# Kernel tuning notes

Measured on AMD Instinct MI355X. Metric: run time of the kernel, lower is better.

## Reference

```python
import jax, jax.numpy as jnp
import numpy as np

GRID = 64
DX = 1.0 / GRID            # grid spacing (buffer dx)
RADIUS = 2.5 * DX          # search_radius = dx * 2.5
CIN, COUT = 16, 16
B, N = 2, 8192
EPS = 1e-12
FOUR_OVER_PI = 4.0 / np.pi


def _safe_sqrt(v):
    return jnp.sqrt(jnp.maximum(v, EPS))


def _sphere_to_cylinder(x, y, z):
    # volume-preserving map: unit ball -> cylinder (radius 1, height 2)
    sq = x * x + y * y + z * z
    norm = _safe_sqrt(sq)
    xy2 = x * x + y * y
    cap = 1.25 * z * z > xy2                      # polar-cap region
    s_cap = jnp.sqrt(3.0 * norm / (norm + jnp.abs(z) + EPS))
    s_side = norm / _safe_sqrt(xy2)
    xc = jnp.where(cap, x * s_cap, x * s_side)
    yc = jnp.where(cap, y * s_cap, y * s_side)
    zc = jnp.where(cap, jnp.sign(z) * norm, 1.5 * z)
    zero = sq <= EPS
    z0 = jnp.zeros_like(x)
    return (jnp.where(zero, z0, xc), jnp.where(zero, z0, yc), jnp.where(zero, z0, zc))


def _cylinder_to_cube(x, y, z):
    # area-preserving disc -> square on the xy cross-section
    xy2 = x * x + y * y
    nxy = _safe_sqrt(xy2)
    xdom = jnp.abs(y) <= jnp.abs(x)
    safe_x = jnp.where(jnp.abs(x) > EPS, x, 1.0)
    safe_y = jnp.where(jnp.abs(y) > EPS, y, 1.0)
    tx = jnp.sign(x) * nxy
    ty = jnp.sign(y) * nxy
    xa, ya = tx, tx * FOUR_OVER_PI * jnp.arctan(y / safe_x)
    xb, yb = ty * FOUR_OVER_PI * jnp.arctan(x / safe_y), ty
    xc = jnp.where(xdom, xa, xb)
    yc = jnp.where(xdom, ya, yb)
    zero = xy2 <= EPS
    z0 = jnp.zeros_like(x)
    return jnp.where(zero, z0, xc), jnp.where(zero, z0, yc), z


def _cconv_forward(input, pos, weights, grid_pos):
    Bb, C, D, H, Wd = input.shape
    Np = pos.shape[1]
    # [B,C,D,H,W] -> [B,D,H,W,C] -> [B,G,C]  (matches permute+view in torch)
    feat = jnp.transpose(input, (0, 2, 3, 4, 1)).reshape(Bb, D * H * Wd, C)
    # fixed 6^3 stencil of candidate grid cells around each point
    off = jnp.arange(6) - 2
    o0, o1, o2 = jnp.meshgrid(off, off, off, indexing='ij')
    offs = jnp.stack([o0, o1, o2], axis=-1).reshape(-1, 3)          # [216,3]
    base = jnp.floor(pos / DX).astype(jnp.int32)                    # [B,N,3]
    cand = base[:, :, None, :] + offs[None, None]                   # [B,N,216,3]
    dims = jnp.array([D, H, Wd])
    in_bounds = jnp.all((cand >= 0) & (cand < dims), axis=-1)       # [B,N,216]
    cc = jnp.clip(cand, 0, dims - 1)
    flat = (cc[..., 0] * H + cc[..., 1]) * Wd + cc[..., 2]          # [B,N,216]
    bidx = jnp.arange(Bb)[:, None, None]
    npos = grid_pos[flat]                                           # [B,N,216,3]
    fg = feat[bidx, flat]                                           # [B,N,216,C]
    rel = npos - pos[:, :, None, :]
    dist2 = jnp.sum(rel * rel, axis=-1)
    valid = in_bounds & (dist2 <= RADIUS * RADIUS)
    # map relative offsets (scaled to the unit ball) to the unit cube
    u = rel / RADIUS
    x, y, z = _sphere_to_cylinder(u[..., 0], u[..., 1], u[..., 2])
    x, y, z = _cylinder_to_cube(x, y, z)
    # linear interpolation of the 3x3x3 kernel, align_corners=True -> coords in [0,2]
    taps = jnp.arange(3, dtype=pos.dtype)
    def hat(c):
        c = jnp.clip((c * 0.5 + 0.5) * 2.0, 0.0, 2.0)
        return jnp.maximum(0.0, 1.0 - jnp.abs(c[..., None] - taps))  # [B,N,216,3]
    w0, w1, w2 = hat(x), hat(y), hat(z)
    w27 = jnp.einsum('bnki,bnkj,bnkl->bnkijl', w0, w1, w2).reshape(Bb, Np, -1, 27)
    w27 = w27 * valid[..., None].astype(w27.dtype)
    # accumulate interpolated features per kernel tap, then apply the kernel
    acc = jnp.einsum('bnkt,bnkc->bntc', w27, fg)                    # [B,N,27,C]
    out = jnp.einsum('bntc,tcd->bnd', acc, weights.reshape(27, C, -1))
    # normalize=True (Open3D default): divide by neighbor count
    count = jnp.sum(valid, axis=-1).astype(out.dtype)
    out = out / jnp.maximum(count, 1.0)[..., None]
    return out


def setup_inputs() -> dict:
    key = jax.random.key(0)
    k1, k2, k3 = jax.random.split(key, 3)
    inp = jax.random.normal(k1, (B, CIN, GRID, GRID, GRID), jnp.float32)
    pos = jax.random.uniform(k2, (B, N, 3), jnp.float32)
    weights = jax.random.normal(k3, (3, 3, 3, CIN, COUT), jnp.float32) * 0.05
    ax = jnp.arange(GRID, dtype=jnp.float32) * DX
    g = jnp.stack(jnp.meshgrid(ax, ax, ax, indexing='ij'), axis=-1).reshape(-1, 3)
    return {"input": inp, "pos": pos, "weights": weights, "grid_pos": g}


def reference(input, pos, weights, grid_pos):
    return _cconv_forward(input, pos, weights, grid_pos)
```

## Files before the change

### kernel.cpp

```cpp
#include <hip/hip_runtime.h>
#include <cstdint>

typedef float v2f __attribute__((ext_vector_type(2)));

namespace {
constexpr int kG = 262144;
constexpr int kB = 2;
constexpr int kN = 8192;
constexpr int kPts = kB * kN;
constexpr float kDX = 1.0f / 64.0f;
constexpr float kRad2 = 0.00152587890625f;
constexpr float kInvRad = 25.6f;
constexpr float kEps = 1e-12f;
constexpr float kFourOverPi = 1.27323954473516268615f;

constexpr int PPB = 4;
constexpr int THREADS = PPB * 64;
constexpr int MAXREC = 96;
constexpr int SLOT = 12;
constexpr int NFLAT = 96;
constexpr int GSTRIDE = MAXREC * SLOT + NFLAT;
}

struct Stencil {
    int v[192];
    constexpr Stencil() : v() {
        int n = 0;
        for (int a = 0; a < 6; ++a)
            for (int b = 0; b < 6; ++b)
                for (int c = 0; c < 6; ++c) {
                    int e = ((a == 0) | (a == 5)) + ((b == 0) | (b == 5)) +
                            ((c == 0) | (c == 5));
                    if (e < 2) { v[n] = a | (b << 8) | (c << 16); ++n; }
                }
        for (; n < 192; ++n) v[n] = 0x7F7F7F;
    }
};
__device__ constexpr Stencil kStencil{};

__device__ __forceinline__ float sgnf(float v) {
    return (v > 0.f) ? 1.f : ((v < 0.f) ? -1.f : 0.f);
}

__global__ __launch_bounds__(256) void transpose_feat_k(const float* __restrict__ in,
                                                        float* __restrict__ feat) {
    int idx = blockIdx.x * 256 + threadIdx.x;
    if (idx >= kB * kG) return;
    int b = idx >> 18;
    int g = idx & (kG - 1);
    float v[16];
#pragma unroll
    for (int c = 0; c < 16; ++c) v[c] = in[((size_t)(b * 16 + c)) * kG + g];
    float4* dst = reinterpret_cast<float4*>(feat + (size_t)idx * 16);
    dst[0] = make_float4(v[0], v[1], v[2], v[3]);
    dst[1] = make_float4(v[4], v[5], v[6], v[7]);
    dst[2] = make_float4(v[8], v[9], v[10], v[11]);
    dst[3] = make_float4(v[12], v[13], v[14], v[15]);
}

template <int USE_FEAT>
__global__ __launch_bounds__(THREADS) void cconv_main(
    const float* __restrict__ input, const float* __restrict__ pos,
    const float* __restrict__ W, const float* __restrict__ feat,
    float* __restrict__ out)
{
    __shared__ __align__(16) float rec[PPB * GSTRIDE];

    const int tid = threadIdx.x;
    const int wv = tid >> 6;
    const int lane = tid & 63;
    const int sg = lane >> 4;
    const int lig = lane & 15;
    const int pt = blockIdx.x * PPB + wv;
    const int b = pt >> 13;

    const float px = pos[pt * 3 + 0];
    const float py = pos[pt * 3 + 1];
    const float pz = pos[pt * 3 + 2];
    const int bx = (int)floorf(px * 64.f);
    const int by = (int)floorf(py * 64.f);
    const int bz = (int)floorf(pz * 64.f);

    float* grec = rec + wv * GSTRIDE;
    int* iflats = reinterpret_cast<int*>(grec + MAXREC * SLOT);
    int nv = 0;

#pragma unroll
    for (int it = 0; it < 3; ++it) {
        int k = it * 64 + lane;
        int pk = kStencil.v[k];
        int a = pk & 0xFF, b1 = (pk >> 8) & 0xFF, c1 = pk >> 16;
        int g0 = bx + a - 2, g1 = by + b1 - 2, g2 = bz + c1 - 2;
        bool inb = (g0 >= 0) & (g0 < 64) & (g1 >= 0) & (g1 < 64) &
                   (g2 >= 0) & (g2 < 64);
        int q0 = min(max(g0, 0), 63);
        int q1 = min(max(g1, 0), 63);
        int q2 = min(max(g2, 0), 63);
        int flat16 = ((q0 * 64 + q1) * 64 + q2) << 4;
        float rx = __fsub_rn((float)q0 * kDX, px);
        float ry = __fsub_rn((float)q1 * kDX, py);
        float rz = __fsub_rn((float)q2 * kDX, pz);
        float d2 = __fadd_rn(__fadd_rn(__fmul_rn(rx, rx), __fmul_rn(ry, ry)),
                             __fmul_rn(rz, rz));
        bool valid = inb && (d2 <= kRad2);
        unsigned long long ball = __ballot(valid);
        if (valid) {
            int slot = nv + __popcll(ball & ((1ull << lane) - 1ull));
            *reinterpret_cast<float4*>(grec + slot * SLOT) =
                make_float4(rx, ry, rz, 0.f);
            iflats[slot] = flat16;
        }
        nv += (int)__popcll(ball);
    }
    __builtin_amdgcn_wave_barrier();

    for (int z = nv + lane; z < MAXREC; z += 64) {
        float4 zf = make_float4(0.f, 0.f, 0.f, 0.f);
        float4* zp = reinterpret_cast<float4*>(grec + z * SLOT);
        zp[0] = zf; zp[1] = zf; zp[2] = zf;
        iflats[z] = 0;
    }
    __builtin_amdgcn_wave_barrier();

    const float* fbp = USE_FEAT ? (feat + (size_t)b * kG * 16)
                                : (input + (size_t)b * 16 * kG);
#define LDF(IDX) (USE_FEAT ? fbp[(size_t)iflats[(IDX)] + lig]                 \
                           : fbp[(size_t)lig * kG + (iflats[(IDX)] >> 4)])
    float fa0 = LDF(sg),      fa1 = LDF(sg + 4);
    float fa2 = LDF(sg + 8),  fa3 = LDF(sg + 12);
    float fb0 = LDF(sg + 16), fb1 = LDF(sg + 20);
    float fb2 = LDF(sg + 24), fb3 = LDF(sg + 28);

    for (int s = lane; s < nv; s += 64) {
        float* rp = grec + s * SLOT;
        float4 rc = *reinterpret_cast<const float4*>(rp);
        float ux = rc.x * kInvRad, uy = rc.y * kInvRad, uz = rc.z * kInvRad;

        float xx = ux * ux, yy = uy * uy, zz = uz * uz;
        float xy2 = xx + yy;
        float sq = xy2 + zz;
        float nrm = __builtin_amdgcn_sqrtf(fmaxf(sq, kEps));
        bool cap = (1.25f * zz > xy2);
        float scap = __builtin_amdgcn_sqrtf(3.f * nrm) *
                     __builtin_amdgcn_rsqf(nrm + fabsf(uz) + kEps);
        float sside = nrm * __builtin_amdgcn_rsqf(fmaxf(xy2, kEps));
        float sc = cap ? scap : sside;
        float xc = ux * sc, yc = uy * sc;
        float zc = cap ? sgnf(uz) * nrm : 1.5f * uz;
        if (sq <= kEps) { xc = 0.f; yc = 0.f; zc = 0.f; }

        float xy2b = xc * xc + yc * yc;
        float nxy = __builtin_amdgcn_sqrtf(fmaxf(xy2b, kEps));
        bool xdom = (fabsf(yc) <= fabsf(xc));
        float num = xdom ? yc : xc;
        float den = xdom ? xc : yc;
        float dsafe = (fabsf(den) > kEps) ? den : 1.0f;
        float r = num * __builtin_amdgcn_rcpf(dsafe);
        float r2 = r * r;
        float at = -0.01172120f;
        at = at * r2 + 0.05265332f;
        at = at * r2 - 0.11643287f;
        at = at * r2 + 0.19354346f;
        at = at * r2 - 0.33262347f;
        at = at * r2 + 0.99997726f;
        at = at * r;
        float tt = sgnf(den) * nxy;
        float g = tt * kFourOverPi * at;
        float xo = xdom ? tt : g;
        float yo = xdom ? g : tt;
        if (xy2b <= kEps) { xo = 0.f; yo = 0.f; }
        float zo = zc;

        float tx = fminf(fmaxf(xo + 1.f, 0.f), 2.f) - 1.f;
        float ty = fminf(fmaxf(yo + 1.f, 0.f), 2.f) - 1.f;
        float tz = fminf(fmaxf(zo + 1.f, 0.f), 2.f) - 1.f;
        float wx0 = fmaxf(0.f, -tx), wx1 = 1.f - fabsf(tx), wx2 = fmaxf(0.f, tx);
        float wy0 = fmaxf(0.f, -ty), wy1 = 1.f - fabsf(ty), wy2 = fmaxf(0.f, ty);
        float wz0 = fmaxf(0.f, -tz), wz1 = 1.f - fabsf(tz);

        float4* rp4 = reinterpret_cast<float4*>(rp);
        rp4[0] = make_float4(wx0 * wy0, wx0 * wy1, wx0 * wy2, wx1 * wy0);
        rp4[1] = make_float4(wx1 * wy1, wx1 * wy2, wx2 * wy0, wx2 * wy1);
        rp4[2] = make_float4(wx2 * wy2, wz0, wz1, 0.f);
    }
    __builtin_amdgcn_wave_barrier();

    v2f az0_01 = {0.f, 0.f}, az1_01 = {0.f, 0.f}, az2_01 = {0.f, 0.f};
    v2f az0_23 = {0.f, 0.f}, az1_23 = {0.f, 0.f}, az2_23 = {0.f, 0.f};
    v2f az0_45 = {0.f, 0.f}, az1_45 = {0.f, 0.f}, az2_45 = {0.f, 0.f};
    v2f az0_67 = {0.f, 0.f}, az1_67 = {0.f, 0.f}, az2_67 = {0.f, 0.f};
    float a8_0 = 0.f, a8_1 = 0.f, a8_2 = 0.f;

    const int R = (nv + 7) & ~7;
    const int F = R >> 4;
    const bool HB = (R & 8) != 0;

#define REC_FMA(S, FV)                                                        \
  {                                                                           \
    const float4* rp4_ = reinterpret_cast<const float4*>(grec + (S) * SLOT);  \
    float4 Wa = rp4_[0], Wb = rp4_[1], Wc = rp4_[2];                          \
    float m0 = Wc.y * (FV), m1 = Wc.z * (FV);                                 \
    float m2 = ((1.f - Wc.y) - Wc.z) * (FV);                                  \
    v2f mz0 = {m0, m0}, mz1 = {m1, m1}, mz2 = {m2, m2};                       \
    v2f p01 = {Wa.x, Wa.y}, p23 = {Wa.z, Wa.w};                               \
    v2f p45 = {Wb.x, Wb.y}, p67 = {Wb.z, Wb.w};                               \
    az0_01 = __builtin_elementwise_fma(p01, mz0, az0_01);                     \
    az1_01 = __builtin_elementwise_fma(p01, mz1, az1_01);                     \
    az2_01 = __builtin_elementwise_fma(p01, mz2, az2_01);                     \
    az0_23 = __builtin_elementwise_fma(p23, mz0, az0_23);                     \
    az1_23 = __builtin_elementwise_fma(p23, mz1, az1_23);                     \
    az2_23 = __builtin_elementwise_fma(p23, mz2, az2_23);                     \
    az0_45 = __builtin_elementwise_fma(p45, mz0, az0_45);                     \
    az1_45 = __builtin_elementwise_fma(p45, mz1, az1_45);                     \
    az2_45 = __builtin_elementwise_fma(p45, mz2, az2_45);                     \
    az0_67 = __builtin_elementwise_fma(p67, mz0, az0_67);                     \
    az1_67 = __builtin_elementwise_fma(p67, mz1, az1_67);                     \
    az2_67 = __builtin_elementwise_fma(p67, mz2, az2_67);                     \
    a8_0 = __builtin_fmaf(Wc.x, m0, a8_0);                                    \
    a8_1 = __builtin_fmaf(Wc.x, m1, a8_1);                                    \
    a8_2 = __builtin_fmaf(Wc.x, m2, a8_2);                                    \
  }

#define P2BODY(KK, F0_, F1_, F2_, F3_)                                        \
  {                                                                           \
    const int rb_ = (KK) * 16 + sg;                                           \
    const bool nxt_ = ((KK) + 2 < F) || ((KK) + 2 == F && HB);                \
    float n0_ = 0.f, n1_ = 0.f, n2_ = 0.f, n3_ = 0.f;                         \
    if (nxt_) {                                                               \
      n0_ = LDF(rb_ + 32); n1_ = LDF(rb_ + 36);                               \
      n2_ = LDF(rb_ + 40); n3_ = LDF(rb_ + 44);                               \
    }                                                                         \
    REC_FMA(rb_, F0_); REC_FMA(rb_ + 4, F1_);                                 \
    if ((KK) < F) { REC_FMA(rb_ + 8, F2_); REC_FMA(rb_ + 12, F3_); }          \
    if (nxt_) { F0_ = n0_; F1_ = n1_; F2_ = n2_; F3_ = n3_; }                 \
  }

     P2BODY(0, fa0, fa1, fa2, fa3)
    if (1 < F || (1 == F && HB)) P2BODY(1, fb0, fb1, fb2, fb3)
    if (2 < F || (2 == F && HB)) P2BODY(2, fa0, fa1, fa2, fa3)
    if (3 < F || (3 == F && HB)) P2BODY(3, fb0, fb1, fb2, fb3)
    if (4 < F || (4 == F && HB)) P2BODY(4, fa0, fa1, fa2, fa3)
    if (5 == F && HB)            P2BODY(5, fb0, fb1, fb2, fb3)

    float acc[28] = {
        az0_01.x, az1_01.x, az2_01.x,
        az0_01.y, az1_01.y, az2_01.y,
        az0_23.x, az1_23.x, az2_23.x,
        az0_23.y, az1_23.y, az2_23.y,
        az0_45.x, az1_45.x, az2_45.x,
        az0_45.y, az1_45.y, az2_45.y,
        az0_67.x, az1_67.x, az2_67.x,
        az0_67.y, az1_67.y, az2_67.y,
        a8_0,     a8_1,     a8_2,
        0.f
    };

    const bool hi32 = (lane >= 32);
    float kp[14];
#pragma unroll
    for (int j = 0; j < 14; ++j) {
        float send = hi32 ? acc[j] : acc[14 + j];
        float recv = __shfl_xor(send, 32);
        kp[j] = (hi32 ? acc[14 + j] : acc[j]) + recv;
    }
    const bool hi16 = (lane & 16) != 0;
    float kk[7];
#pragma unroll
    for (int j = 0; j < 7; ++j) {
        float send = hi16 ? kp[j] : kp[7 + j];
        float recv = __shfl_xor(send, 16);
        kk[j] = (hi16 ? kp[7 + j] : kp[j]) + recv;
    }

    float partial[16];
#pragma unroll
    for (int d = 0; d < 16; ++d) partial[d] = 0.f;
    const float* wbase = W + (sg * 7) * 256 + lig * 16;
#pragma unroll
    for (int j = 0; j < 7; ++j) {
        if (sg * 7 + j < 27) {
            const float4* wr = reinterpret_cast<const float4*>(wbase + j * 256);
            float4 a0 = wr[0], a1 = wr[1], a2 = wr[2], a3 = wr[3];
            float at_ = kk[j];
            partial[0]  += at_ * a0.x; partial[1]  += at_ * a0.y;
            partial[2]  += at_ * a0.z; partial[3]  += at_ * a0.w;
            partial[4]  += at_ * a1.x; partial[5]  += at_ * a1.y;
            partial[6]  += at_ * a1.z; partial[7]  += at_ * a1.w;
            partial[8]  += at_ * a2.x; partial[9]  += at_ * a2.y;
            partial[10] += at_ * a2.z; partial[11] += at_ * a2.w;
            partial[12] += at_ * a3.x; partial[13] += at_ * a3.y;
            partial[14] += at_ * a3.z; partial[15] += at_ * a3.w;
        }
    }

#pragma unroll
    for (int half = 8; half >= 1; half >>= 1) {
        bool up = (lig & half) != 0;
#pragma unroll
        for (int j = 0; j < half; ++j) {
            float send = up ? partial[j] : partial[j + half];
            float recv = __shfl_xor(send, half);
            partial[j] = (up ? partial[j + half] : partial[j]) + recv;
        }
    }
    float res = partial[0];
    res += __shfl_xor(res, 16);
    res += __shfl_xor(res, 32);
    res = res / fmaxf((float)nv, 1.f);
    if (lane < 16) out[(size_t)pt * 16 + lig] = res;
#undef LDF
#undef REC_FMA
#undef P2BODY
}

extern "C" void kernel_launch(void* const* d_in, const int* in_sizes, int n_in,
                              void* d_out, int out_size, void* d_ws, size_t ws_size,
                              hipStream_t stream) {
    const float* input = (const float*)d_in[0];
    const float* pos   = (const float*)d_in[1];
    const float* W     = (const float*)d_in[2];
    float* out  = (float*)d_out;
    float* feat = (float*)d_ws;

    const size_t feat_bytes = (size_t)kB * kG * 16 * sizeof(float);
    int use_feat = (d_ws != nullptr && ws_size >= feat_bytes) ? 1 : 0;

    if (use_feat) {
        transpose_feat_k<<<(kB * kG + 255) / 256, 256, 0, stream>>>(input, feat);
        cconv_main<1><<<kPts / PPB, THREADS, 0, stream>>>(input, pos, W, feat, out);
    } else {
        cconv_main<0><<<kPts / PPB, THREADS, 0, stream>>>(input, pos, W, feat, out);
    }
}
```

Baseline: 73.83 us.

## Remap lanes to 8 cells x 8 channel-pairs with v2f loads and reductions

Changes the per-wave thread mapping from 4 cells x 16 channels to 8 cells x 8 channel pairs. Each lane now loads two adjacent channels as a v2f and accumulates 27 taps for both with packed FMAs. The cross-lane reduction tree and the final weight contraction are rewritten to match, using v2f shuffles and channel-pair weight loads. This aims to halve the number of record passes per cell and make better use of packed math, at the cost of more accumulator registers (54 floats) and a more complex reduction with more shuffles.

```diff
diff --git a/kernel.cpp b/kernel.cpp
--- a/kernel.cpp
+++ b/kernel.cpp
@@ -42,6 +42,13 @@
     return (v > 0.f) ? 1.f : ((v < 0.f) ? -1.f : 0.f);
 }
 
+__device__ __forceinline__ v2f shfl2(v2f v, int m) {
+    v2f r;
+    r.x = __shfl_xor(v.x, m);
+    r.y = __shfl_xor(v.y, m);
+    return r;
+}
+
 __global__ __launch_bounds__(256) void transpose_feat_k(const float* __restrict__ in,
                                                         float* __restrict__ feat) {
     int idx = blockIdx.x * 256 + threadIdx.x;
@@ -69,8 +76,6 @@
     const int tid = threadIdx.x;
     const int wv = tid >> 6;
     const int lane = tid & 63;
-    const int sg = lane >> 4;
-    const int lig = lane & 15;
     const int pt = blockIdx.x * PPB + wv;
     const int b = pt >> 13;
 
@@ -122,14 +127,21 @@
     }
     __builtin_amdgcn_wave_barrier();
 
+    const int cell = lane >> 3;
+    const int cg = lane & 7;
+
     const float* fbp = USE_FEAT ? (feat + (size_t)b * kG * 16)
                                 : (input + (size_t)b * 16 * kG);
-#define LDF(IDX) (USE_FEAT ? fbp[(size_t)iflats[(IDX)] + lig]                 \
-                           : fbp[(size_t)lig * kG + (iflats[(IDX)] >> 4)])
-    float fa0 = LDF(sg),      fa1 = LDF(sg + 4);
-    float fa2 = LDF(sg + 8),  fa3 = LDF(sg + 12);
-    float fb0 = LDF(sg + 16), fb1 = LDF(sg + 20);
-    float fb2 = LDF(sg + 24), fb3 = LDF(sg + 28);
+#define LDF2v(FL)                                                             \
+    (USE_FEAT                                                                 \
+         ? *reinterpret_cast<const v2f*>(fbp + (size_t)(FL) + 2 * cg)         \
+         : (v2f){fbp[(size_t)(2 * cg) * kG + ((FL) >> 4)],                    \
+                 fbp[(size_t)(2 * cg + 1) * kG + ((FL) >> 4)]})
+
+    v2f fA = LDF2v(iflats[cell]);
+    v2f fB = LDF2v(iflats[8 + cell]);
+    v2f fC = LDF2v(iflats[16 + cell]);
+    v2f fD = LDF2v(iflats[24 + cell]);
 
     for (int s = lane; s < nv; s += 64) {
         float* rp = grec + s * SLOT;
@@ -185,131 +197,142 @@
     }
     __builtin_amdgcn_wave_barrier();
 
-    v2f az0_01 = {0.f, 0.f}, az1_01 = {0.f, 0.f}, az2_01 = {0.f, 0.f};
-    v2f az0_23 = {0.f, 0.f}, az1_23 = {0.f, 0.f}, az2_23 = {0.f, 0.f};
-    v2f az0_45 = {0.f, 0.f}, az1_45 = {0.f, 0.f}, az2_45 = {0.f, 0.f};
-    v2f az0_67 = {0.f, 0.f}, az1_67 = {0.f, 0.f}, az2_67 = {0.f, 0.f};
-    float a8_0 = 0.f, a8_1 = 0.f, a8_2 = 0.f;
-
-    const int R = (nv + 7) & ~7;
-    const int F = R >> 4;
-    const bool HB = (R & 8) != 0;
-
-#define REC_FMA(S, FV)                                                        \
+    v2f acc[32];
+#pragma unroll
+    for (int t = 0; t < 32; ++t) acc[t] = (v2f){0.f, 0.f};
+
+#define REC_FMA2(RPTR, FV)                                                    \
   {                                                                           \
-    const float4* rp4_ = reinterpret_cast<const float4*>(grec + (S) * SLOT);  \
+    const float4* rp4_ = reinterpret_cast<const float4*>(RPTR);               \
     float4 Wa = rp4_[0], Wb = rp4_[1], Wc = rp4_[2];                          \
-    float m0 = Wc.y * (FV), m1 = Wc.z * (FV);                                 \
-    float m2 = ((1.f - Wc.y) - Wc.z) * (FV);                                  \
-    v2f mz0 = {m0, m0}, mz1 = {m1, m1}, mz2 = {m2, m2};                       \
-    v2f p01 = {Wa.x, Wa.y}, p23 = {Wa.z, Wa.w};                               \
-    v2f p45 = {Wb.x, Wb.y}, p67 = {Wb.z, Wb.w};                               \
-    az0_01 = __builtin_elementwise_fma(p01, mz0, az0_01);                     \
-    az1_01 = __builtin_elementwise_fma(p01, mz1, az1_01);                     \
-    az2_01 = __builtin_elementwise_fma(p01, mz2, az2_01);                     \
-    az0_23 = __builtin_elementwise_fma(p23, mz0, az0_23);                     \
-    az1_23 = __builtin_elementwise_fma(p23, mz1, az1_23);                     \
-    az2_23 = __builtin_elementwise_fma(p23, mz2, az2_23);                     \
-    az0_45 = __builtin_elementwise_fma(p45, mz0, az0_45);                     \
-    az1_45 = __builtin_elementwise_fma(p45, mz1, az1_45);                     \
-    az2_45 = __builtin_elementwise_fma(p45, mz2, az2_45);                     \
-    az0_67 = __builtin_elementwise_fma(p67, mz0, az0_67);                     \
-    az1_67 = __builtin_elementwise_fma(p67, mz1, az1_67);                     \
-    az2_67 = __builtin_elementwise_fma(p67, mz2, az2_67);                     \
-    a8_0 = __builtin_fmaf(Wc.x, m0, a8_0);                                    \
-    a8_1 = __builtin_fmaf(Wc.x, m1, a8_1);                                    \
-    a8_2 = __builtin_fmaf(Wc.x, m2, a8_2);                                    \
+    v2f m0 = (v2f){Wc.y, Wc.y} * (FV);                                        \
+    v2f m1 = (v2f){Wc.z, Wc.z} * (FV);                                        \
+    float wz2_ = (1.f - Wc.y) - Wc.z;                                         \
+    v2f m2 = (v2f){wz2_, wz2_} * (FV);                                        \
+    acc[0]  = __builtin_elementwise_fma((v2f){Wa.x, Wa.x}, m0, acc[0]);       \
+    acc[1]  = __builtin_elementwise_fma((v2f){Wa.x, Wa.x}, m1, acc[1]);       \
+    acc[2]  = __builtin_elementwise_fma((v2f){Wa.x, Wa.x}, m2, acc[2]);       \
+    acc[3]  = __builtin_elementwise_fma((v2f){Wa.y, Wa.y}, m0, acc[3]);       \
+    acc[4]  = __builtin_elementwise_fma((v2f){Wa.y, Wa.y}, m1, acc[4]);       \
+    acc[5]  = __builtin_elementwise_fma((v2f){Wa.y, Wa.y}, m2, acc[5]);       \
+    acc[6]  = __builtin_elementwise_fma((v2f){Wa.z, Wa.z}, m0, acc[6]);       \
+    acc[7]  = __builtin_elementwise_fma((v2f){Wa.z, Wa.z}, m1, acc[7]);       \
+    acc[8]  = __builtin_elementwise_fma((v2f){Wa.z, Wa.z}, m2, acc[8]);       \
+    acc[9]  = __builtin_elementwise_fma((v2f){Wa.w, Wa.w}, m0, acc[9]);       \
+    acc[10] = __builtin_elementwise_fma((v2f){Wa.w, Wa.w}, m1, acc[10]);      \
+    acc[11] = __builtin_elementwise_fma((v2f){Wa.w, Wa.w}, m2, acc[11]);      \
+    acc[12] = __builtin_elementwise_fma((v2f){Wb.x, Wb.x}, m0, acc[12]);      \
+    acc[13] = __builtin_elementwise_fma((v2f){Wb.x, Wb.x}, m1, acc[13]);      \
+    acc[14] = __builtin_elementwise_fma((v2f){Wb.x, Wb.x}, m2, acc[14]);      \
+    acc[15] = __builtin_elementwise_fma((v2f){Wb.y, Wb.y}, m0, acc[15]);      \
+    acc[16] = __builtin_elementwise_fma((v2f){Wb.y, Wb.y}, m1, acc[16]);      \
+    acc[17] = __builtin_elementwise_fma((v2f){Wb.y, Wb.y}, m2, acc[17]);      \
+    acc[18] = __builtin_elementwise_fma((v2f){Wb.z, Wb.z}, m0, acc[18]);      \
+    acc[19] = __builtin_elementwise_fma((v2f){Wb.z, Wb.z}, m1, acc[19]);      \
+    acc[20] = __builtin_elementwise_fma((v2f){Wb.z, Wb.z}, m2, acc[20]);      \
+    acc[21] = __builtin_elementwise_fma((v2f){Wb.w, Wb.w}, m0, acc[21]);      \
+    acc[22] = __builtin_elementwise_fma((v2f){Wb.w, Wb.w}, m1, acc[22]);      \
+    acc[23] = __builtin_elementwise_fma((v2f){Wb.w, Wb.w}, m2, acc[23]);      \
+    acc[24] = __builtin_elementwise_fma((v2f){Wc.x, Wc.x}, m0, acc[24]);      \
+    acc[25] = __builtin_elementwise_fma((v2f){Wc.x, Wc.x}, m1, acc[25]);      \
+    acc[26] = __builtin_elementwise_fma((v2f){Wc.x, Wc.x}, m2, acc[26]);      \
   }
 
-#define P2BODY(KK, F0_, F1_, F2_, F3_)                                        \
-  {                                                                           \
-    const int rb_ = (KK) * 16 + sg;                                           \
-    const bool nxt_ = ((KK) + 2 < F) || ((KK) + 2 == F && HB);                \
-    float n0_ = 0.f, n1_ = 0.f, n2_ = 0.f, n3_ = 0.f;                         \
-    if (nxt_) {                                                               \
-      n0_ = LDF(rb_ + 32); n1_ = LDF(rb_ + 36);                               \
-      n2_ = LDF(rb_ + 40); n3_ = LDF(rb_ + 44);                               \
-    }                                                                         \
-    REC_FMA(rb_, F0_); REC_FMA(rb_ + 4, F1_);                                 \
-    if ((KK) < F) { REC_FMA(rb_ + 8, F2_); REC_FMA(rb_ + 12, F3_); }          \
-    if (nxt_) { F0_ = n0_; F1_ = n1_; F2_ = n2_; F3_ = n3_; }                 \
+#define P2BODY(KK, FCUR)                                                      \
+  if ((KK) * 8 < nv) {                                                        \
+    v2f fn_ = FCUR;                                                           \
+    if (((KK) + 4) * 8 < nv) fn_ = LDF2v(iflats[((KK) + 4) * 8 + cell]);      \
+    REC_FMA2(grec + ((KK) * 8 + cell) * SLOT, FCUR);                          \
+    FCUR = fn_;                                                               \
   }
 
-     P2BODY(0, fa0, fa1, fa2, fa3)
-    if (1 < F || (1 == F && HB)) P2BODY(1, fb0, fb1, fb2, fb3)
-    if (2 < F || (2 == F && HB)) P2BODY(2, fa0, fa1, fa2, fa3)
-    if (3 < F || (3 == F && HB)) P2BODY(3, fb0, fb1, fb2, fb3)
-    if (4 < F || (4 == F && HB)) P2BODY(4, fa0, fa1, fa2, fa3)
-    if (5 == F && HB)            P2BODY(5, fb0, fb1, fb2, fb3)
-
-    float acc[28] = {
-        az0_01.x, az1_01.x, az2_01.x,
-        az0_01.y, az1_01.y, az2_01.y,
-        az0_23.x, az1_23.x, az2_23.x,
-        az0_23.y, az1_23.y, az2_23.y,
-        az0_45.x, az1_45.x, az2_45.x,
-        az0_45.y, az1_45.y, az2_45.y,
-        az0_67.x, az1_67.x, az2_67.x,
-        az0_67.y, az1_67.y, az2_67.y,
-        a8_0,     a8_1,     a8_2,
-        0.f
-    };
-
-    const bool hi32 = (lane >= 32);
-    float kp[14];
-#pragma unroll
-    for (int j = 0; j < 14; ++j) {
-        float send = hi32 ? acc[j] : acc[14 + j];
-        float recv = __shfl_xor(send, 32);
-        kp[j] = (hi32 ? acc[14 + j] : acc[j]) + recv;
-    }
-    const bool hi16 = (lane & 16) != 0;
-    float kk[7];
-#pragma unroll
-    for (int j = 0; j < 7; ++j) {
-        float send = hi16 ? kp[j] : kp[7 + j];
-        float recv = __shfl_xor(send, 16);
-        kk[j] = (hi16 ? kp[7 + j] : kp[j]) + recv;
-    }
-
-    float partial[16];
-#pragma unroll
-    for (int d = 0; d < 16; ++d) partial[d] = 0.f;
-    const float* wbase = W + (sg * 7) * 256 + lig * 16;
-#pragma unroll
-    for (int j = 0; j < 7; ++j) {
-        if (sg * 7 + j < 27) {
-            const float4* wr = reinterpret_cast<const float4*>(wbase + j * 256);
-            float4 a0 = wr[0], a1 = wr[1], a2 = wr[2], a3 = wr[3];
-            float at_ = kk[j];
-            partial[0]  += at_ * a0.x; partial[1]  += at_ * a0.y;
-            partial[2]  += at_ * a0.z; partial[3]  += at_ * a0.w;
-            partial[4]  += at_ * a1.x; partial[5]  += at_ * a1.y;
-            partial[6]  += at_ * a1.z; partial[7]  += at_ * a1.w;
-            partial[8]  += at_ * a2.x; partial[9]  += at_ * a2.y;
-            partial[10] += at_ * a2.z; partial[11] += at_ * a2.w;
-            partial[12] += at_ * a3.x; partial[13] += at_ * a3.y;
-            partial[14] += at_ * a3.z; partial[15] += at_ * a3.w;
+    P2BODY(0, fA)  P2BODY(1, fB)  P2BODY(2, fC)  P2BODY(3, fD)
+    P2BODY(4, fA)  P2BODY(5, fB)  P2BODY(6, fC)  P2BODY(7, fD)
+    P2BODY(8, fA)  P2BODY(9, fB)  P2BODY(10, fC) P2BODY(11, fD)
+
+    const int b2 = (lane >> 2) & 1;
+    const int b3 = (lane >> 3) & 1;
+    const int b4 = (lane >> 4) & 1;
+    const int b5 = (lane >> 5) & 1;
+
+    v2f kp[16];
+#pragma unroll
+    for (int j = 0; j < 16; ++j) {
+        v2f send = b3 ? acc[j] : acc[16 + j];
+        v2f keep = b3 ? acc[16 + j] : acc[j];
+        kp[j] = keep + shfl2(send, 8);
+    }
+    v2f kq[8];
+#pragma unroll
+    for (int j = 0; j < 8; ++j) {
+        v2f send = b4 ? kp[j] : kp[8 + j];
+        v2f keep = b4 ? kp[8 + j] : kp[j];
+        kq[j] = keep + shfl2(send, 16);
+    }
+    v2f kkv[4];
+#pragma unroll
+    for (int j = 0; j < 4; ++j) {
+        v2f send = b5 ? kq[j] : kq[4 + j];
+        v2f keep = b5 ? kq[4 + j] : kq[j];
+        kkv[j] = keep + shfl2(send, 32);
+    }
+
+    const int tbase = 16 * b3 + 8 * b4 + 4 * b5;
+    const int c0 = 2 * cg;
+    v2f part[8];
+#pragma unroll
+    for (int p = 0; p < 8; ++p) part[p] = (v2f){0.f, 0.f};
+#pragma unroll
+    for (int j = 0; j < 4; ++j) {
+        int t = tbase + j;
+        int tc = (t < 27) ? t : 26;
+        const float4* w0 = reinterpret_cast<const float4*>(W + tc * 256 + c0 * 16);
+        float k0 = kkv[j].x, k1 = kkv[j].y;
+        v2f vk0 = (v2f){k0, k0}, vk1 = (v2f){k1, k1};
+#pragma unroll
+        for (int q = 0; q < 4; ++q) {
+            float4 a = w0[q];
+            float4 c = w0[q + 4];
+            part[2 * q] = __builtin_elementwise_fma(vk0, (v2f){a.x, a.y}, part[2 * q]);
+            part[2 * q] = __builtin_elementwise_fma(vk1, (v2f){c.x, c.y}, part[2 * q]);
+            part[2 * q + 1] = __builtin_elementwise_fma(vk0, (v2f){a.z, a.w}, part[2 * q + 1]);
+            part[2 * q + 1] = __builtin_elementwise_fma(vk1, (v2f){c.z, c.w}, part[2 * q + 1]);
         }
     }
 
-#pragma unroll
-    for (int half = 8; half >= 1; half >>= 1) {
-        bool up = (lig & half) != 0;
-#pragma unroll
-        for (int j = 0; j < half; ++j) {
-            float send = up ? partial[j] : partial[j + half];
-            float recv = __shfl_xor(send, half);
-            partial[j] = (up ? partial[j + half] : partial[j]) + recv;
-        }
-    }
-    float res = partial[0];
-    res += __shfl_xor(res, 16);
-    res += __shfl_xor(res, 32);
+    v2f s4[4];
+#pragma unroll
+    for (int j = 0; j < 4; ++j) {
+        v2f send = b2 ? part[j] : part[4 + j];
+        v2f keep = b2 ? part[4 + j] : part[j];
+        s4[j] = keep + shfl2(send, 4);
+    }
+    v2f s2[2];
+#pragma unroll
+    for (int j = 0; j < 2; ++j) {
+        v2f send = b3 ? s4[j] : s4[2 + j];
+        v2f keep = b3 ? s4[2 + j] : s4[j];
+        s2[j] = keep + shfl2(send, 8);
+    }
+    v2f s1;
+    {
+        v2f send = b4 ? s2[0] : s2[1];
+        v2f keep = b4 ? s2[1] : s2[0];
+        s1 = keep + shfl2(send, 16);
+    }
+    float res;
+    {
+        float send = b5 ? s1.x : s1.y;
+        float keep = b5 ? s1.y : s1.x;
+        res = keep + __shfl_xor(send, 32);
+    }
+    res += __shfl_xor(res, 2);
+    res += __shfl_xor(res, 1);
     res = res / fmaxf((float)nv, 1.f);
-    if (lane < 16) out[(size_t)pt * 16 + lig] = res;
-#undef LDF
-#undef REC_FMA
+    const int d = 8 * b2 + 4 * b3 + 2 * b4 + b5;
+    if ((lane & 3) == 0) out[(size_t)pt * 16 + d] = res;
+#undef LDF2v
+#undef REC_FMA2
 #undef P2BODY
 }
 
```

Result: slower. 96.20 us (+30.3%).
